# Performance work log

Measured on AMD Instinct MI355X. Metric: run time of the kernel, lower is better.

Reference implementation:

```python
import jax, jax.numpy as jnp
import numpy as np
from jax import lax

B, C, N_WIN, H, W = 64, 3, 232, 64, 64
TSTEPS = 8
CHUNK = N_WIN // TSTEPS            # 29
KD, KH, KW = 4, 2, 2
SD, SH, SW = 2, 2, 2
DP = (CHUNK - KD) // SD + 1        # 13
HP = (H - KH) // SH + 1            # 32
WP = (W - KW) // SW + 1            # 32
IN_DIM = HP * WP                   # 1024
H0, H1, H2 = 512, 512, 256
CD = C * DP                        # 39
FEAT = CD * H2                     # 9984
N_CLASSES = 4
BETA = 0.9
THR = 0.5
SLOPE = 25.0                       # snntorch fast_sigmoid default slope

@jax.custom_vjp
def spike(v):
    return (v > 0).astype(v.dtype)

def _spike_fwd(v):
    return spike(v), v

def _spike_bwd(v, g):
    return (g / (SLOPE * jnp.abs(v) + 1.0) ** 2,)

spike.defvjp(_spike_fwd, _spike_bwd)

def lif(cur, mem, beta, thr):
    # snntorch Leaky, reset-by-subtraction; reset flag computed from previous mem and detached
    reset = lax.stop_gradient((mem > thr).astype(mem.dtype))
    mem_new = beta * mem + cur - reset * thr
    spk = spike(mem_new - thr)
    return spk, mem_new

def setup_inputs():
    key = jax.random.key(0)
    ks = jax.random.split(key, 5)
    def lin(k, out_f, in_f):
        kw, kb = jax.random.split(k)
        lim = 1.0 / np.sqrt(in_f)
        Wm = jax.random.uniform(kw, (out_f, in_f), jnp.float32, -lim, lim)
        bm = jax.random.uniform(kb, (out_f,), jnp.float32, -lim, lim)
        return Wm, bm
    x = jax.random.normal(ks[0], (B, C, N_WIN, H, W), jnp.float32)
    W_in, b_in = lin(ks[1], H0, IN_DIM)
    W_h1, b_h1 = lin(ks[2], H1, H0)
    W_h2, b_h2 = lin(ks[3], H2, H1)
    W_out, b_out = lin(ks[4], N_CLASSES, FEAT)
    return {"x": x, "W_in": W_in, "b_in": b_in, "W_h1": W_h1, "b_h1": b_h1,
            "W_h2": W_h2, "b_h2": b_h2, "W_out": W_out, "b_out": b_out}

def reference(x, W_in, b_in, W_h1, b_h1, W_h2, b_h2, W_out, b_out):
    # split into timestep chunks: (T, B, C, CHUNK, H, W)
    xt = x.reshape(B, C, TSTEPS, CHUNK, H, W).transpose(2, 0, 1, 3, 4, 5)
    # avg_pool3d over (CHUNK, H, W) per timestep, VALID padding (matches nn.AvgPool3d)
    win = (1, 1, 1, KD, KH, KW)
    st = (1, 1, 1, SD, SH, SW)
    pooled = lax.reduce_window(xt, jnp.float32(0), lax.add, win, st, "VALID")
    pooled = pooled / (KD * KH * KW)               # (T, B, C, DP, HP, WP)
    xt = pooled.reshape(TSTEPS, B, CD, IN_DIM)

    m_in = jnp.zeros((B, CD, H0), jnp.float32)
    m_h1 = jnp.zeros((B, CD, H1), jnp.float32)
    m_h2 = jnp.zeros((B, CD, H2), jnp.float32)
    m_out = jnp.zeros((B, N_CLASSES), jnp.float32)

    def step(carry, x_t):
        m_in, m_h1, m_h2, m_out = carry
        cur = x_t @ W_in.T + b_in
        s, m_in = lif(cur, m_in, BETA, THR)
        cur = s @ W_h1.T + b_h1
        s, m_h1 = lif(cur, m_h1, BETA, THR)
        cur = s @ W_h2.T + b_h2
        s, m_h2 = lif(cur, m_h2, BETA, THR)
        cur = s.reshape(B, FEAT) @ W_out.T + b_out
        s_out, m_out = lif(cur, m_out, BETA, 1.0)   # output LIF uses threshold=1.0
        return (m_in, m_h1, m_h2, m_out), s_out

    _, spk_rec = lax.scan(step, (m_in, m_h1, m_h2, m_out), xt)
    return spk_rec                                  # (TSTEPS, B, N_CLASSES)
```

## Files before the change

### kernel.cpp

```cpp
#include <hip/hip_runtime.h>
#include <hip/hip_bf16.h>

#define B_   64
#define C_   3
#define NWIN 232
#define TSTEPS 8
#define CHUNK 29
#define DP_  13
#define HP_  32
#define WP_  32
#define IN_DIM 1024
#define H0_  512
#define H1_  512
#define H2_  256
#define CD_  39
#define M_   (B_*CD_)
#define FEAT 9984
#define NCLS 4

__global__ __launch_bounds__(256) void pool_kernel(const float* __restrict__ x,
                                                   float* __restrict__ xt, int t) {
    int tid = blockIdx.x * 256 + threadIdx.x;
    int wp = tid & 31;
    int hp = (tid >> 5) & 31;
    int v  = tid >> 10;
    int c  = v % 3;
    int b  = v / 3;

    const float* base = x + (((size_t)(b * 3 + c) * NWIN + t * CHUNK) * 64 + hp * 2) * 64 + wp * 2;

    float acc[DP_];
#pragma unroll
    for (int d = 0; d < DP_; d++) acc[d] = 0.f;

#pragma unroll
    for (int f = 0; f < CHUNK; f++) {
        const float* p = base + (size_t)f * 4096;
        float2 r0 = *(const float2*)p;
        float2 r1 = *(const float2*)(p + 64);
        float fs = (r0.x + r0.y) + (r1.x + r1.y);
        int dplo = (f >= 3) ? ((f - 2) >> 1) : 0;
        int dphi = (f >> 1) > 12 ? 12 : (f >> 1);
#pragma unroll
        for (int d = dplo; d <= dphi; d++) acc[d] += fs;
    }

    float* o = xt + (size_t)(b * CD_ + c * DP_) * IN_DIM + hp * 32 + wp;
#pragma unroll
    for (int d = 0; d < DP_; d++) o[(size_t)d * IN_DIM] = acc[d] * (1.f / 16.f);
}

#define LDSS 68
__global__ __launch_bounds__(256) void gemm_lif(const float* __restrict__ A,
                                                const float* __restrict__ W,
                                                const float* __restrict__ bias,
                                                float* __restrict__ mem,
                                                float* __restrict__ spk,
                                                int N, int K, float thr) {
    __shared__ float As[16][LDSS];
    __shared__ float Ws[16][LDSS];

    int tid = threadIdx.x;
    int bm = blockIdx.y;
    int bn = blockIdx.x;

    int lrow = tid >> 2;
    int lkq  = tid & 3;

    const float* Ap = A + (size_t)(bm * 64 + lrow) * K + lkq * 4;
    const float* Wp = W + (size_t)(bn * 64 + lrow) * K + lkq * 4;

    int tm = tid & 15;
    int tn = tid >> 4;

    float acc[4][4];
#pragma unroll
    for (int i = 0; i < 4; i++)
#pragma unroll
        for (int j = 0; j < 4; j++) acc[i][j] = 0.f;

    for (int kt = 0; kt < K; kt += 16) {
        float4 a = *(const float4*)(Ap + kt);
        float4 w = *(const float4*)(Wp + kt);
        As[lkq * 4 + 0][lrow] = a.x;
        As[lkq * 4 + 1][lrow] = a.y;
        As[lkq * 4 + 2][lrow] = a.z;
        As[lkq * 4 + 3][lrow] = a.w;
        Ws[lkq * 4 + 0][lrow] = w.x;
        Ws[lkq * 4 + 1][lrow] = w.y;
        Ws[lkq * 4 + 2][lrow] = w.z;
        Ws[lkq * 4 + 3][lrow] = w.w;
        __syncthreads();
#pragma unroll
        for (int k = 0; k < 16; k++) {
            float4 av = *(const float4*)&As[k][tm * 4];
            float4 bv = *(const float4*)&Ws[k][tn * 4];
            float aa[4] = {av.x, av.y, av.z, av.w};
            float bb[4] = {bv.x, bv.y, bv.z, bv.w};
#pragma unroll
            for (int i = 0; i < 4; i++)
#pragma unroll
                for (int j = 0; j < 4; j++) acc[i][j] += aa[i] * bb[j];
        }
        __syncthreads();
    }

#pragma unroll
    for (int i = 0; i < 4; i++) {
        int m = bm * 64 + tm * 4 + i;
#pragma unroll
        for (int j = 0; j < 4; j++) {
            int n = bn * 64 + tn * 4 + j;
            float cur = acc[i][j] + bias[n];
            size_t idx = (size_t)m * N + n;
            float mv = mem[idx];
            float reset = (mv > thr) ? 1.f : 0.f;
            float mn = 0.9f * mv + cur - reset * thr;
            mem[idx] = mn;
            spk[idx] = ((mn - thr) > 0.f) ? 1.f : 0.f;
        }
    }
}

__global__ __launch_bounds__(256) void out_kernel(const float* __restrict__ s2,
                                                  const float* __restrict__ Wout,
                                                  const float* __restrict__ bout,
                                                  float* __restrict__ m_out,
                                                  float* __restrict__ out, int t) {
    int b = blockIdx.x;
    int tid = threadIdx.x;
    const float* s = s2 + (size_t)b * FEAT;
    float a0 = 0.f, a1 = 0.f, a2 = 0.f, a3 = 0.f;
    for (int k = tid; k < FEAT; k += 256) {
        float a = s[k];
        a0 += a * Wout[k];
        a1 += a * Wout[FEAT + k];
        a2 += a * Wout[2 * FEAT + k];
        a3 += a * Wout[3 * FEAT + k];
    }
    __shared__ float red[4][256];
    red[0][tid] = a0; red[1][tid] = a1; red[2][tid] = a2; red[3][tid] = a3;
    __syncthreads();
    for (int sft = 128; sft > 0; sft >>= 1) {
        if (tid < sft) {
#pragma unroll
            for (int n = 0; n < 4; n++) red[n][tid] += red[n][tid + sft];
        }
        __syncthreads();
    }
    if (tid < 4) {
        float cur = red[tid][0] + bout[tid];
        float mv = m_out[b * 4 + tid];
        float reset = (mv > 1.0f) ? 1.f : 0.f;
        float mn = 0.9f * mv + cur - reset * 1.0f;
        m_out[b * 4 + tid] = mn;
        out[t * (B_ * NCLS) + b * 4 + tid] = ((mn - 1.0f) > 0.f) ? 1.f : 0.f;
    }
}

extern "C" void kernel_launch(void* const* d_in, const int* in_sizes, int n_in,
                              void* d_out, int out_size, void* d_ws, size_t ws_size,
                              hipStream_t stream) {
    const float* x     = (const float*)d_in[0];
    const float* W_in  = (const float*)d_in[1];
    const float* b_in  = (const float*)d_in[2];
    const float* W_h1  = (const float*)d_in[3];
    const float* b_h1  = (const float*)d_in[4];
    const float* W_h2  = (const float*)d_in[5];
    const float* b_h2  = (const float*)d_in[6];
    const float* W_out = (const float*)d_in[7];
    const float* b_out = (const float*)d_in[8];

    float* ws  = (float*)d_ws;
    float* xt  = ws;
    float* s0  = xt  + (size_t)M_ * IN_DIM;
    float* s1  = s0  + (size_t)M_ * H0_;
    float* s2  = s1  + (size_t)M_ * H1_;
    float* m_in = s2  + (size_t)M_ * H2_;
    float* m_h1 = m_in + (size_t)M_ * H0_;
    float* m_h2 = m_h1 + (size_t)M_ * H1_;
    float* m_o  = m_h2 + (size_t)M_ * H2_;

    size_t memBytes = ((size_t)M_ * (H0_ + H1_ + H2_) + B_ * NCLS) * sizeof(float);
    hipMemsetAsync(m_in, 0, memBytes, stream);

    for (int t = 0; t < TSTEPS; t++) {
        pool_kernel<<<(B_ * C_ * HP_ * WP_) / 256, 256, 0, stream>>>(x, xt, t);
        gemm_lif<<<dim3(H0_ / 64, M_ / 64), 256, 0, stream>>>(xt, W_in, b_in, m_in, s0, H0_, IN_DIM, 0.5f);
        gemm_lif<<<dim3(H1_ / 64, M_ / 64), 256, 0, stream>>>(s0, W_h1, b_h1, m_h1, s1, H1_, H0_, 0.5f);
        gemm_lif<<<dim3(H2_ / 64, M_ / 64), 256, 0, stream>>>(s1, W_h2, b_h2, m_h2, s2, H2_, H1_, 0.5f);
        out_kernel<<<B_, 256, 0, stream>>>(s2, W_out, b_out, m_o, (float*)d_out, t);
    }
}
```

Measured before the change: 2.175 ms.

## Use bf16 MFMA with hi/lo split GEMMs and batch pooling up front

The three FP32 SIMT GEMMs are replaced by MFMA bf16 16x16x32 kernels. Each operand is split into bf16 hi and lo parts, and the K dimension is laid out as concatenated hi/lo segments (3K for the input layer, 2K for the hidden layers) so that one GEMM computes a near-FP32 product. Spikes are exactly 0 or 1, so they are stored as bf16 and duplicated for the hidden layers. Pooling for all timesteps now runs in one launch, with rows padded to 2560, and weights are split on every call. This trades extra K-length and preprocessing for matrix-core throughput, and it risks small precision differences that could flip spikes.

```diff
diff --git a/kernel.cpp b/kernel.cpp
--- a/kernel.cpp
+++ b/kernel.cpp
@@ -15,17 +15,48 @@
 #define H2_  256
 #define CD_  39
 #define M_   (B_*CD_)
+#define MPAD 2560
 #define FEAT 9984
 #define NCLS 4
-
-__global__ __launch_bounds__(256) void pool_kernel(const float* __restrict__ x,
-                                                   float* __restrict__ xt, int t) {
-    int tid = blockIdx.x * 256 + threadIdx.x;
-    int wp = tid & 31;
-    int hp = (tid >> 5) & 31;
-    int v  = tid >> 10;
-    int c  = v % 3;
-    int b  = v / 3;
+#define BETA 0.9f
+
+typedef unsigned short ushort_t;
+typedef short s16x8 __attribute__((ext_vector_type(8)));
+typedef float f32x4 __attribute__((ext_vector_type(4)));
+
+__device__ __forceinline__ ushort_t f2bf(float f) {
+    unsigned int u = __float_as_uint(f);
+    unsigned int r = u + 0x7FFFu + ((u >> 16) & 1u);
+    return (ushort_t)(r >> 16);
+}
+__device__ __forceinline__ float bf2f(ushort_t h) {
+    return __uint_as_float(((unsigned int)h) << 16);
+}
+
+__global__ __launch_bounds__(256) void split_w(const float* __restrict__ W,
+                                               ushort_t* __restrict__ out,
+                                               int N, int K, int dup) {
+    int i = blockIdx.x * 256 + threadIdx.x;
+    if (i >= N * K) return;
+    int n = i / K, k = i - n * K;
+    float w = W[i];
+    ushort_t hi = f2bf(w);
+    ushort_t lo = f2bf(w - bf2f(hi));
+    size_t rb = (size_t)n * (size_t)(dup ? 3 * K : 2 * K);
+    out[rb + k] = hi;
+    out[rb + K + k] = lo;
+    if (dup) out[rb + 2 * K + k] = hi;
+}
+
+__global__ __launch_bounds__(256) void pool_all(const float* __restrict__ x,
+                                                ushort_t* __restrict__ xt2) {
+    int v = blockIdx.x * 256 + threadIdx.x;
+    int wp = v & 31;
+    int hp = (v >> 5) & 31;
+    int u = v >> 10;
+    int c = u % 3; u /= 3;
+    int b = u % 64;
+    int t = u / 64;
 
     const float* base = x + (((size_t)(b * 3 + c) * NWIN + t * CHUNK) * 64 + hp * 2) * 64 + wp * 2;
 
@@ -45,94 +76,115 @@
         for (int d = dplo; d <= dphi; d++) acc[d] += fs;
     }
 
-    float* o = xt + (size_t)(b * CD_ + c * DP_) * IN_DIM + hp * 32 + wp;
-#pragma unroll
-    for (int d = 0; d < DP_; d++) o[(size_t)d * IN_DIM] = acc[d] * (1.f / 16.f);
-}
-
-#define LDSS 68
-__global__ __launch_bounds__(256) void gemm_lif(const float* __restrict__ A,
-                                                const float* __restrict__ W,
+    ushort_t* o = xt2 + (size_t)t * MPAD * 3072
+                      + (size_t)(b * CD_ + c * DP_) * 3072 + hp * 32 + wp;
+#pragma unroll
+    for (int d = 0; d < DP_; d++) {
+        float a = acc[d] * (1.f / 16.f);
+        ushort_t hi = f2bf(a);
+        ushort_t lo = f2bf(a - bf2f(hi));
+        o[(size_t)d * 3072] = hi;
+        o[(size_t)d * 3072 + 1024] = hi;
+        o[(size_t)d * 3072 + 2048] = lo;
+    }
+}
+
+__global__ __launch_bounds__(256) void gemm_lif(const ushort_t* __restrict__ A,
+                                                const ushort_t* __restrict__ W2,
                                                 const float* __restrict__ bias,
                                                 float* __restrict__ mem,
-                                                float* __restrict__ spk,
-                                                int N, int K, float thr) {
-    __shared__ float As[16][LDSS];
-    __shared__ float Ws[16][LDSS];
+                                                ushort_t* __restrict__ spk,
+                                                int K, int N, int spkStride,
+                                                int dupOff, float thr) {
+    __shared__ __align__(16) ushort_t Als[8 * 512];
+    __shared__ __align__(16) ushort_t Wls[8 * 512];
 
     int tid = threadIdx.x;
+    int bn = blockIdx.x;
     int bm = blockIdx.y;
-    int bn = blockIdx.x;
-
-    int lrow = tid >> 2;
-    int lkq  = tid & 3;
-
-    const float* Ap = A + (size_t)(bm * 64 + lrow) * K + lkq * 4;
-    const float* Wp = W + (size_t)(bn * 64 + lrow) * K + lkq * 4;
-
-    int tm = tid & 15;
-    int tn = tid >> 4;
-
-    float acc[4][4];
-#pragma unroll
-    for (int i = 0; i < 4; i++)
-#pragma unroll
-        for (int j = 0; j < 4; j++) acc[i][j] = 0.f;
-
-    for (int kt = 0; kt < K; kt += 16) {
-        float4 a = *(const float4*)(Ap + kt);
-        float4 w = *(const float4*)(Wp + kt);
-        As[lkq * 4 + 0][lrow] = a.x;
-        As[lkq * 4 + 1][lrow] = a.y;
-        As[lkq * 4 + 2][lrow] = a.z;
-        As[lkq * 4 + 3][lrow] = a.w;
-        Ws[lkq * 4 + 0][lrow] = w.x;
-        Ws[lkq * 4 + 1][lrow] = w.y;
-        Ws[lkq * 4 + 2][lrow] = w.z;
-        Ws[lkq * 4 + 3][lrow] = w.w;
+    int rowBase = bm * 64;
+    int colBase = bn * 64;
+
+    int w = tid >> 6;
+    int lane = tid & 63;
+    int wm = w >> 1;
+    int wn = w & 1;
+
+    int sr = tid >> 3;
+    int scg = tid & 7;
+    int skb = scg >> 2;
+    int slq = scg & 3;
+
+    f32x4 acc[2][2];
+#pragma unroll
+    for (int i = 0; i < 2; i++)
+#pragma unroll
+        for (int j = 0; j < 2; j++) acc[i][j] = (f32x4)(0.f);
+
+    for (int kt = 0; kt < K; kt += 64) {
+#pragma unroll
+        for (int p = 0; p < 2; p++) {
+            int r = sr + p * 32;
+            int fl = (r & 15) + 16 * slq;
+            int fr = (r >> 4) * 2 + skb;
+            uint4 va = *(const uint4*)(A + (size_t)(rowBase + r) * K + kt + scg * 8);
+            uint4 vw = *(const uint4*)(W2 + (size_t)(colBase + r) * K + kt + scg * 8);
+            *(uint4*)(&Als[fr * 512 + fl * 8]) = va;
+            *(uint4*)(&Wls[fr * 512 + fl * 8]) = vw;
+        }
         __syncthreads();
 #pragma unroll
-        for (int k = 0; k < 16; k++) {
-            float4 av = *(const float4*)&As[k][tm * 4];
-            float4 bv = *(const float4*)&Ws[k][tn * 4];
-            float aa[4] = {av.x, av.y, av.z, av.w};
-            float bb[4] = {bv.x, bv.y, bv.z, bv.w};
-#pragma unroll
-            for (int i = 0; i < 4; i++)
-#pragma unroll
-                for (int j = 0; j < 4; j++) acc[i][j] += aa[i] * bb[j];
+        for (int kb = 0; kb < 2; kb++) {
+            s16x8 a0 = *(const s16x8*)(&Als[((wm * 2 + 0) * 2 + kb) * 512 + lane * 8]);
+            s16x8 a1 = *(const s16x8*)(&Als[((wm * 2 + 1) * 2 + kb) * 512 + lane * 8]);
+            s16x8 b0 = *(const s16x8*)(&Wls[((wn * 2 + 0) * 2 + kb) * 512 + lane * 8]);
+            s16x8 b1 = *(const s16x8*)(&Wls[((wn * 2 + 1) * 2 + kb) * 512 + lane * 8]);
+            acc[0][0] = __builtin_amdgcn_mfma_f32_16x16x32_bf16(a0, b0, acc[0][0], 0, 0, 0);
+            acc[0][1] = __builtin_amdgcn_mfma_f32_16x16x32_bf16(a0, b1, acc[0][1], 0, 0, 0);
+            acc[1][0] = __builtin_amdgcn_mfma_f32_16x16x32_bf16(a1, b0, acc[1][0], 0, 0, 0);
+            acc[1][1] = __builtin_amdgcn_mfma_f32_16x16x32_bf16(a1, b1, acc[1][1], 0, 0, 0);
         }
         __syncthreads();
     }
 
-#pragma unroll
-    for (int i = 0; i < 4; i++) {
-        int m = bm * 64 + tm * 4 + i;
-#pragma unroll
-        for (int j = 0; j < 4; j++) {
-            int n = bn * 64 + tn * 4 + j;
-            float cur = acc[i][j] + bias[n];
-            size_t idx = (size_t)m * N + n;
-            float mv = mem[idx];
-            float reset = (mv > thr) ? 1.f : 0.f;
-            float mn = 0.9f * mv + cur - reset * thr;
-            mem[idx] = mn;
-            spk[idx] = ((mn - thr) > 0.f) ? 1.f : 0.f;
-        }
-    }
-}
-
-__global__ __launch_bounds__(256) void out_kernel(const float* __restrict__ s2,
+    int ccol = lane & 15;
+    int crow = (lane >> 4) * 4;
+#pragma unroll
+    for (int mt = 0; mt < 2; mt++) {
+#pragma unroll
+        for (int nt = 0; nt < 2; nt++) {
+            int col = colBase + wn * 32 + nt * 16 + ccol;
+            int row0 = rowBase + wm * 32 + mt * 16 + crow;
+            float bv = bias[col];
+#pragma unroll
+            for (int reg = 0; reg < 4; reg++) {
+                int r = row0 + reg;
+                float cur = acc[mt][nt][reg] + bv;
+                size_t mi = (size_t)r * N + col;
+                float mv = mem[mi];
+                float reset = (mv > thr) ? 1.f : 0.f;
+                float mn = BETA * mv + cur - reset * thr;
+                mem[mi] = mn;
+                ushort_t s = ((mn - thr) > 0.f) ? (ushort_t)0x3F80 : (ushort_t)0;
+                size_t si = (size_t)r * spkStride + col;
+                spk[si] = s;
+                if (dupOff) spk[si + dupOff] = s;
+            }
+        }
+    }
+}
+
+__global__ __launch_bounds__(256) void out_kernel(const ushort_t* __restrict__ s2,
                                                   const float* __restrict__ Wout,
                                                   const float* __restrict__ bout,
                                                   float* __restrict__ m_out,
                                                   float* __restrict__ out, int t) {
     int b = blockIdx.x;
     int tid = threadIdx.x;
-    const float* s = s2 + (size_t)b * FEAT;
+    const ushort_t* s = s2 + (size_t)b * CD_ * H2_;
     float a0 = 0.f, a1 = 0.f, a2 = 0.f, a3 = 0.f;
     for (int k = tid; k < FEAT; k += 256) {
-        float a = s[k];
+        float a = bf2f(s[k]);
         a0 += a * Wout[k];
         a1 += a * Wout[FEAT + k];
         a2 += a * Wout[2 * FEAT + k];
@@ -152,7 +204,7 @@
         float cur = red[tid][0] + bout[tid];
         float mv = m_out[b * 4 + tid];
         float reset = (mv > 1.0f) ? 1.f : 0.f;
-        float mn = 0.9f * mv + cur - reset * 1.0f;
+        float mn = BETA * mv + cur - reset * 1.0f;
         m_out[b * 4 + tid] = mn;
         out[t * (B_ * NCLS) + b * 4 + tid] = ((mn - 1.0f) > 0.f) ? 1.f : 0.f;
     }
@@ -171,24 +223,36 @@
     const float* W_out = (const float*)d_in[7];
     const float* b_out = (const float*)d_in[8];
 
-    float* ws  = (float*)d_ws;
-    float* xt  = ws;
-    float* s0  = xt  + (size_t)M_ * IN_DIM;
-    float* s1  = s0  + (size_t)M_ * H0_;
-    float* s2  = s1  + (size_t)M_ * H1_;
-    float* m_in = s2  + (size_t)M_ * H2_;
-    float* m_h1 = m_in + (size_t)M_ * H0_;
-    float* m_h2 = m_h1 + (size_t)M_ * H1_;
-    float* m_o  = m_h2 + (size_t)M_ * H2_;
-
-    size_t memBytes = ((size_t)M_ * (H0_ + H1_ + H2_) + B_ * NCLS) * sizeof(float);
+    char* p = (char*)d_ws;
+    ushort_t* xt2  = (ushort_t*)p; p += (size_t)TSTEPS * MPAD * 3072 * 2;
+    ushort_t* W2i  = (ushort_t*)p; p += (size_t)H0_ * 3072 * 2;
+    ushort_t* W2h1 = (ushort_t*)p; p += (size_t)H1_ * 1024 * 2;
+    ushort_t* W2h2 = (ushort_t*)p; p += (size_t)H2_ * 1024 * 2;
+    ushort_t* s0   = (ushort_t*)p; p += (size_t)MPAD * 1024 * 2;
+    ushort_t* s1   = (ushort_t*)p; p += (size_t)MPAD * 1024 * 2;
+    ushort_t* s2   = (ushort_t*)p; p += (size_t)MPAD * 256 * 2;
+    float* m_in = (float*)p; p += (size_t)MPAD * H0_ * 4;
+    float* m_h1 = (float*)p; p += (size_t)MPAD * H1_ * 4;
+    float* m_h2 = (float*)p; p += (size_t)MPAD * H2_ * 4;
+    float* m_o  = (float*)p; p += (size_t)B_ * NCLS * 4;
+
+    size_t memBytes = ((size_t)MPAD * (H0_ + H1_ + H2_) + B_ * NCLS) * sizeof(float);
     hipMemsetAsync(m_in, 0, memBytes, stream);
 
+    split_w<<<(H0_ * IN_DIM + 255) / 256, 256, 0, stream>>>(W_in, W2i, H0_, IN_DIM, 1);
+    split_w<<<(H1_ * H0_ + 255) / 256, 256, 0, stream>>>(W_h1, W2h1, H1_, H0_, 0);
+    split_w<<<(H2_ * H1_ + 255) / 256, 256, 0, stream>>>(W_h2, W2h2, H2_, H1_, 0);
+
+    pool_all<<<(TSTEPS * B_ * C_ * HP_ * WP_) / 256, 256, 0, stream>>>(x, xt2);
+
     for (int t = 0; t < TSTEPS; t++) {
-        pool_kernel<<<(B_ * C_ * HP_ * WP_) / 256, 256, 0, stream>>>(x, xt, t);
-        gemm_lif<<<dim3(H0_ / 64, M_ / 64), 256, 0, stream>>>(xt, W_in, b_in, m_in, s0, H0_, IN_DIM, 0.5f);
-        gemm_lif<<<dim3(H1_ / 64, M_ / 64), 256, 0, stream>>>(s0, W_h1, b_h1, m_h1, s1, H1_, H0_, 0.5f);
-        gemm_lif<<<dim3(H2_ / 64, M_ / 64), 256, 0, stream>>>(s1, W_h2, b_h2, m_h2, s2, H2_, H1_, 0.5f);
+        const ushort_t* At = xt2 + (size_t)t * MPAD * 3072;
+        gemm_lif<<<dim3(H0_ / 64, MPAD / 64), 256, 0, stream>>>(
+            At, W2i, b_in, m_in, s0, 3072, H0_, 1024, 512, 0.5f);
+        gemm_lif<<<dim3(H1_ / 64, MPAD / 64), 256, 0, stream>>>(
+            s0, W2h1, b_h1, m_h1, s1, 1024, H1_, 1024, 512, 0.5f);
+        gemm_lif<<<dim3(H2_ / 64, MPAD / 64), 256, 0, stream>>>(
+            s1, W2h2, b_h2, m_h2, s2, 1024, H2_, 256, 0, 0.5f);
         out_kernel<<<B_, 256, 0, stream>>>(s2, W_out, b_out, m_o, (float*)d_out, t);
     }
 }
```

Measured after the change: 2.103 ms. -3.3%, faster.
